# Kernel optimization log

Measured on AMD Instinct MI355X. Metric: run time of the kernel, lower is better.

The kernel has to match this reference:

```python
import jax, jax.numpy as jnp
import numpy as np

B, C, N = 8, 64, 4096
K, M = 20, 8  # neighbors, num_kernel
OUT_C = 64
NEG_SLOPE = 0.2


def setup_inputs() -> dict:
    key = jax.random.key(0)
    k1, k2, k3, k4, k5, k6 = jax.random.split(key, 6)
    x = jax.random.normal(k1, (B, 3, N), dtype=jnp.float32)
    feature = jax.random.normal(k2, (B, C, N), dtype=jnp.float32)
    neigh_indexs = jax.random.randint(k3, (B, N, K), 0, N, dtype=jnp.int64)
    kernels = jax.random.normal(k4, (3, M), dtype=jnp.float32)
    conv_w = jax.random.normal(k5, (OUT_C, C * M), dtype=jnp.float32) * (1.0 / np.sqrt(C * M))
    conv_b = jax.random.normal(k6, (OUT_C,), dtype=jnp.float32) * 0.01
    return {"x": x, "feature": feature, "neigh_indexs": neigh_indexs,
            "kernels": kernels, "conv_w": conv_w, "conv_b": conv_b}


def reference(x, feature, neigh_indexs, kernels, conv_w, conv_b):
    b, c, n = feature.shape
    k = K
    m = kernels.shape[1]
    idx = neigh_indexs[:, :, :k]  # dilation=1 slice, (B,N,K)
    bidx = jnp.arange(b)[:, None, None]

    xt = jnp.transpose(x, (0, 2, 1))            # (B,N,3)
    x_neighs = xt[bidx, idx]                    # (B,N,K,3) irregular gather
    x_rel = x_neighs - x_neighs[:, :, :1, :]    # relative coords to first neighbor

    # kernel projection + one_padding buffer (zeros with [0,0]=1)
    one_pad = jnp.zeros((k, m), dtype=x.dtype).at[0, 0].set(1.0)
    permatrix = jnp.einsum('bnkc,cm->bnkm', x_rel, kernels) + one_pad
    # topkmax: stable softmax over the neighbor axis (soft assignment of
    # neighbors to each of the m kernel slots)
    permatrix = jax.nn.softmax(permatrix, axis=2)  # (B,N,K,M)

    ft = jnp.transpose(feature, (0, 2, 1))      # (B,N,C)
    f_neighs = ft[bidx, idx]                    # (B,N,K,C)
    # feats (B*N,C,K) @ permatrix (B*N,K,M) -> (B*N,C,M); flatten C-major
    agg = jnp.einsum('bnkc,bnkm->bncm', f_neighs, permatrix).reshape(b, n, c * m)

    # BasicConv: 1x1 conv == dense over channel dim, then LeakyReLU(0.2)
    out = agg @ conv_w.T + conv_b               # (B,N,out_c)
    out = jax.nn.leaky_relu(out, NEG_SLOPE)
    out = jnp.transpose(out, (0, 2, 1))         # (B,out_c,N)
    return out + feature                        # residual since in_c == out_c
```

## Files before the change

kernel.cpp:

```cpp
#include <hip/hip_runtime.h>
#include <hip/hip_bf16.h>

#define BB 8
#define CC 64
#define NNN 4096
#define KK 20
#define MM 8
#define OC 64
#define CM 512

typedef __attribute__((ext_vector_type(8))) short bf16x8;
typedef __attribute__((ext_vector_type(4))) float f32x4;
typedef __attribute__((ext_vector_type(2))) float f32x2;

__device__ __forceinline__ unsigned short f2bf(float f) {
    union { float f; unsigned int u; } v; v.f = f;
    unsigned int u = v.u;
    return (unsigned short)((u + 0x7FFFu + ((u >> 16) & 1u)) >> 16);
}
__device__ __forceinline__ unsigned int pack2bf(float a, float b) {
    union { __hip_bfloat162 h; unsigned int u; } pk;
    pk.h = __float22bfloat162_rn(make_float2(a, b));
    return pk.u;
}
__device__ __forceinline__ float bfhi2f(unsigned int u) {
    union { unsigned int u; float f; } v; v.u = u & 0xffff0000u; return v.f;
}
__device__ __forceinline__ float bflo2f(unsigned int u) {
    union { unsigned int u; float f; } v; v.u = u << 16; return v.f;
}

__global__ __launch_bounds__(256) void prep_kernel(const float* __restrict__ x,
                                                   const float* __restrict__ feature,
                                                   const float* __restrict__ kern,
                                                   const float* __restrict__ conv_w,
                                                   unsigned short* __restrict__ ftr,
                                                   unsigned short* __restrict__ Wb,
                                                   float* __restrict__ proj) {
    int blk = blockIdx.x;
    int t = threadIdx.x;
    if (blk < 512) {
        __shared__ float tile[64 * 65];
        int b = blk & 7;
        int n0 = (blk >> 3) << 6;
        const float* fb = feature + b * (CC * NNN);
        #pragma unroll
        for (int s = 0; s < 16; ++s) {
            int i = t + s * 256;
            int c = i >> 6, nn = i & 63;
            tile[c * 65 + nn] = fb[c * NNN + n0 + nn];
        }
        __syncthreads();
        unsigned short* fo = ftr + b * (NNN * CC) + n0 * CC;
        #pragma unroll
        for (int s = 0; s < 16; ++s) {
            int i = t + s * 256;
            int n = i >> 6, cc = i & 63;
            fo[n * CC + cc] = f2bf(tile[cc * 65 + n]);
        }
    } else if (blk < 516) {
        int base = (blk - 512) * 8192;
        #pragma unroll
        for (int s = 0; s < 32; ++s) {
            int i = base + t + s * 256;
            int o = i >> 9, col = i & 511;
            int j = col >> 6, cL = (col >> 3) & 7, m = col & 7;
            int cm = ((cL * 8 + j) << 3) | m;
            Wb[i] = f2bf(conv_w[(o << 9) | cm]);
        }
    } else {
        int pb = blk - 516;
        int b = pb >> 2;
        int nb = (pb & 3) << 10;
        const float* xb = x + b * (3 * NNN);
        float k0[MM], k1[MM], k2[MM];
        #pragma unroll
        for (int m = 0; m < MM; ++m) {
            k0[m] = kern[m]; k1[m] = kern[MM + m]; k2[m] = kern[2 * MM + m];
        }
        #pragma unroll
        for (int s = 0; s < 4; ++s) {
            int n = nb + s * 256 + t;
            float x0 = xb[n], x1 = xb[NNN + n], x2 = xb[2 * NNN + n];
            float pr[MM];
            #pragma unroll
            for (int m = 0; m < MM; ++m)
                pr[m] = x0 * k0[m] + x1 * k1[m] + x2 * k2[m];
            float* pp = proj + ((size_t)b * NNN + n) * MM;
            *(float4*)pp = make_float4(pr[0], pr[1], pr[2], pr[3]);
            *(float4*)(pp + 4) = make_float4(pr[4], pr[5], pr[6], pr[7]);
        }
    }
}

__global__ __launch_bounds__(256, 3) void aggr_kernel(const int* __restrict__ nidx,
                                                      const float* __restrict__ proj,
                                                      const unsigned short* __restrict__ ftr,
                                                      unsigned short* __restrict__ agg) {
    __shared__ unsigned short perm[4][8 * 168];

    int t = threadIdx.x, w = t >> 6, l = t & 63;
    int p = l >> 3, h = l & 7;
    int blk = blockIdx.x;
    int b = blk & 7;
    int n0 = ((blk >> 3) << 5) + (w << 3);
    int rowp = b * NNN + n0 + p;

    int id[KK];
    {
        const int4* nb4 = (const int4*)(nidx + rowp * KK);
        #pragma unroll
        for (int s = 0; s < 5; ++s) {
            int4 v = nb4[s];
            id[s * 4 + 0] = v.x; id[s * 4 + 1] = v.y;
            id[s * 4 + 2] = v.z; id[s * 4 + 3] = v.w;
        }
    }

    const float* pj = proj + (size_t)b * NNN * MM;
    float pv[KK];
    #pragma unroll
    for (int k = 0; k < KK; ++k) pv[k] = pj[id[k] * MM + h];

    const unsigned short* fb = ftr + (size_t)b * NNN * CC;
    uint4 fr[KK];
    #pragma unroll
    for (int k = 0; k < KK; ++k)
        fr[k] = *(const uint4*)(fb + (size_t)id[k] * CC + h * 8);

    float pbase = pv[0];
    #pragma unroll
    for (int k = 0; k < KK; ++k) pv[k] -= pbase;
    if (h == 0) pv[0] += 1.0f;
    float mx = pv[0];
    #pragma unroll
    for (int k = 1; k < KK; ++k) mx = fmaxf(mx, pv[k]);
    float sum = 0.f;
    #pragma unroll
    for (int k = 0; k < KK; ++k) { pv[k] = __expf(pv[k] - mx); sum += pv[k]; }
    float inv = 1.0f / sum;

    {
        unsigned short* pw = perm[w] + p * 168;
        #pragma unroll
        for (int k = 0; k < KK; ++k) pw[k * 8 + h] = f2bf(pv[k] * inv);
    }
    __asm__ __volatile__("s_waitcnt lgkmcnt(0)" ::: "memory");

    f32x2 acc[4][MM];
    #pragma unroll
    for (int d = 0; d < 4; ++d)
        #pragma unroll
        for (int m = 0; m < MM; ++m) acc[d][m] = (f32x2){0.f, 0.f};

    const unsigned short* prd = perm[w] + p * 168;
    #pragma unroll
    for (int k = 0; k < KK; ++k) {
        union { bf16x8 v; unsigned int u[4]; } pm8;
        pm8.v = *(const bf16x8*)(prd + k * 8);
        float pm[MM];
        #pragma unroll
        for (int d = 0; d < 4; ++d) {
            pm[2 * d] = bflo2f(pm8.u[d]);
            pm[2 * d + 1] = bfhi2f(pm8.u[d]);
        }
        const unsigned int* fu = (const unsigned int*)&fr[k];
        f32x2 fv[4];
        #pragma unroll
        for (int d = 0; d < 4; ++d)
            fv[d] = (f32x2){bflo2f(fu[d]), bfhi2f(fu[d])};
        #pragma unroll
        for (int m = 0; m < MM; ++m) {
            f32x2 pmm = {pm[m], pm[m]};
            #pragma unroll
            for (int d = 0; d < 4; ++d)
                acc[d][m] += fv[d] * pmm;
        }
    }

    unsigned short* ag = agg + (size_t)rowp * CM;
    #pragma unroll
    for (int jj = 0; jj < 8; ++jj) {
        int d = jj >> 1;
        unsigned int d0, d1, d2, d3;
        if ((jj & 1) == 0) {
            d0 = pack2bf(acc[d][0].x, acc[d][1].x);
            d1 = pack2bf(acc[d][2].x, acc[d][3].x);
            d2 = pack2bf(acc[d][4].x, acc[d][5].x);
            d3 = pack2bf(acc[d][6].x, acc[d][7].x);
        } else {
            d0 = pack2bf(acc[d][0].y, acc[d][1].y);
            d1 = pack2bf(acc[d][2].y, acc[d][3].y);
            d2 = pack2bf(acc[d][4].y, acc[d][5].y);
            d3 = pack2bf(acc[d][6].y, acc[d][7].y);
        }
        uint4 vv = make_uint4(d0, d1, d2, d3);
        *(uint4*)(ag + jj * 64 + h * 8) = vv;
    }
}

__global__ __launch_bounds__(128, 4) void gemm_kernel(const unsigned short* __restrict__ agg,
                                                      const unsigned short* __restrict__ Wb,
                                                      const float* __restrict__ conv_b,
                                                      const float* __restrict__ feature,
                                                      float* __restrict__ out) {
    int t = threadIdx.x, w = t >> 6, l = t & 63;
    int blk = blockIdx.x;
    int b = blk & 7;
    int g = blk >> 3;
    int Wid = g * 2 + w;
    int og = Wid & 1;
    int pg = Wid >> 1;
    int n0 = pg << 5;
    int oA = og * 32 + (l & 15), oB = oA + 16;
    int q = l >> 4;
    int r0 = b * NNN + n0 + (l & 15);

    const unsigned short* a0p = agg + (size_t)r0 * CM + q * 8;
    const unsigned short* a1p = a0p + 16 * CM;
    const unsigned short* w0p = Wb + (size_t)oA * CM + q * 8;
    const unsigned short* w1p = Wb + (size_t)oB * CM + q * 8;

    const float* fA = feature + ((size_t)b * CC + oA) * NNN + n0 + q * 4;
    const float* fB = feature + ((size_t)b * CC + oB) * NNN + n0 + q * 4;
    float4 resA0 = *(const float4*)fA;
    float4 resA1 = *(const float4*)(fA + 16);
    float4 resB0 = *(const float4*)fB;
    float4 resB1 = *(const float4*)(fB + 16);
    float biasA = conv_b[oA], biasB = conv_b[oB];

    f32x4 d00 = {0,0,0,0}, d01 = {0,0,0,0}, d10 = {0,0,0,0}, d11 = {0,0,0,0};
    #pragma unroll
    for (int s = 0; s < 16; ++s) {
        bf16x8 a0 = *(const bf16x8*)(a0p + s * 32);
        bf16x8 a1 = *(const bf16x8*)(a1p + s * 32);
        bf16x8 w0f = *(const bf16x8*)(w0p + s * 32);
        bf16x8 w1f = *(const bf16x8*)(w1p + s * 32);
        d00 = __builtin_amdgcn_mfma_f32_16x16x32_bf16(a0, w0f, d00, 0, 0, 0);
        d01 = __builtin_amdgcn_mfma_f32_16x16x32_bf16(a0, w1f, d01, 0, 0, 0);
        d10 = __builtin_amdgcn_mfma_f32_16x16x32_bf16(a1, w0f, d10, 0, 0, 0);
        d11 = __builtin_amdgcn_mfma_f32_16x16x32_bf16(a1, w1f, d11, 0, 0, 0);
    }

    float* opA = out + ((size_t)b * OC + oA) * NNN + n0 + q * 4;
    float* opB = out + ((size_t)b * OC + oB) * NNN + n0 + q * 4;
    float4 rA0, rA1, rB0, rB1;
    #pragma unroll
    for (int r = 0; r < 4; ++r) {
        float v;
        v = d00[r] + biasA; v = v > 0.f ? v : v * 0.2f; ((float*)&rA0)[r] = v + ((const float*)&resA0)[r];
        v = d10[r] + biasA; v = v > 0.f ? v : v * 0.2f; ((float*)&rA1)[r] = v + ((const float*)&resA1)[r];
        v = d01[r] + biasB; v = v > 0.f ? v : v * 0.2f; ((float*)&rB0)[r] = v + ((const float*)&resB0)[r];
        v = d11[r] + biasB; v = v > 0.f ? v : v * 0.2f; ((float*)&rB1)[r] = v + ((const float*)&resB1)[r];
    }
    *(float4*)opA = rA0;
    *(float4*)(opA + 16) = rA1;
    *(float4*)opB = rB0;
    *(float4*)(opB + 16) = rB1;
}

extern "C" void kernel_launch(void* const* d_in, const int* in_sizes, int n_in,
                              void* d_out, int out_size, void* d_ws, size_t ws_size,
                              hipStream_t stream) {
    const float* x        = (const float*)d_in[0];
    const float* feature  = (const float*)d_in[1];
    const int*   nidx     = (const int*)d_in[2];
    const float* kern     = (const float*)d_in[3];
    const float* conv_w   = (const float*)d_in[4];
    const float* conv_b   = (const float*)d_in[5];
    float* out = (float*)d_out;

    char* ws = (char*)d_ws;
    unsigned short* ftr  = (unsigned short*)ws;
    unsigned short* Wb   = (unsigned short*)(ws + (4u << 20));
    float*          proj = (float*)(ws + (4u << 20) + (64u << 10));
    unsigned short* agg  = (unsigned short*)(ws + (5u << 20) + (64u << 10));

    prep_kernel<<<548, 256, 0, stream>>>(x, feature, kern, conv_w, ftr, Wb, proj);
    aggr_kernel<<<1024, 256, 0, stream>>>(nidx, proj, ftr, agg);
    gemm_kernel<<<1024, 128, 0, stream>>>(agg, Wb, conv_b, feature, out);
}
```

Before: 120.1 us.

## Fuse neighbor aggregation and output GEMM into one kernel via LDS

Merges the aggregation and MFMA GEMM kernels so each 128-thread block aggregates 16 points into shared memory and immediately runs the 1x1 conv, removing the global round trip of the bf16 aggregate buffer and one launch. It also drops the pbase subtraction (softmax is shift-invariant), restores natural weight column ordering with a matching LDS layout, and double-buffers the neighbor feature gathers in groups of four to cut register pressure. In exchange each block has more serial work and a block barrier, and the weight rows are re-read by every block.

```diff
diff --git a/kernel.cpp b/kernel.cpp
--- a/kernel.cpp
+++ b/kernel.cpp
@@ -8,6 +8,9 @@
 #define MM 8
 #define OC 64
 #define CM 512
+#define PST 168
+#define AST 520
+#define REGW 5504
 
 typedef __attribute__((ext_vector_type(8))) short bf16x8;
 typedef __attribute__((ext_vector_type(4))) float f32x4;
@@ -63,10 +66,7 @@
         #pragma unroll
         for (int s = 0; s < 32; ++s) {
             int i = base + t + s * 256;
-            int o = i >> 9, col = i & 511;
-            int j = col >> 6, cL = (col >> 3) & 7, m = col & 7;
-            int cm = ((cL * 8 + j) << 3) | m;
-            Wb[i] = f2bf(conv_w[(o << 9) | cm]);
+            Wb[i] = f2bf(conv_w[i]);
         }
     } else {
         int pb = blk - 516;
@@ -93,22 +93,30 @@
     }
 }
 
-__global__ __launch_bounds__(256, 3) void aggr_kernel(const int* __restrict__ nidx,
-                                                      const float* __restrict__ proj,
-                                                      const unsigned short* __restrict__ ftr,
-                                                      unsigned short* __restrict__ agg) {
-    __shared__ unsigned short perm[4][8 * 168];
+__global__ __launch_bounds__(128, 3) void main_kernel(
+    const int* __restrict__ nidx,
+    const float* __restrict__ proj,
+    const unsigned short* __restrict__ ftr,
+    const unsigned short* __restrict__ Wb,
+    const float* __restrict__ conv_b,
+    const float* __restrict__ feature,
+    float* __restrict__ out)
+{
+    __shared__ __align__(16) unsigned short sm[2 * REGW];
 
     int t = threadIdx.x, w = t >> 6, l = t & 63;
     int p = l >> 3, h = l & 7;
     int blk = blockIdx.x;
     int b = blk & 7;
-    int n0 = ((blk >> 3) << 5) + (w << 3);
-    int rowp = b * NNN + n0 + p;
+    int n0 = (blk >> 3) << 4;
+    int rowp = b * NNN + n0 + w * 8 + p;
+
+    unsigned short* permW = sm + w * REGW;
+    unsigned short* aggW  = sm + w * REGW + 8 * PST;
 
     int id[KK];
     {
-        const int4* nb4 = (const int4*)(nidx + rowp * KK);
+        const int4* nb4 = (const int4*)(nidx + (size_t)rowp * KK);
         #pragma unroll
         for (int s = 0; s < 5; ++s) {
             int4 v = nb4[s];
@@ -123,14 +131,11 @@
     for (int k = 0; k < KK; ++k) pv[k] = pj[id[k] * MM + h];
 
     const unsigned short* fb = ftr + (size_t)b * NNN * CC;
-    uint4 fr[KK];
-    #pragma unroll
-    for (int k = 0; k < KK; ++k)
-        fr[k] = *(const uint4*)(fb + (size_t)id[k] * CC + h * 8);
-
-    float pbase = pv[0];
-    #pragma unroll
-    for (int k = 0; k < KK; ++k) pv[k] -= pbase;
+    uint4 frA[4], frB[4];
+    #pragma unroll
+    for (int j = 0; j < 4; ++j)
+        frA[j] = *(const uint4*)(fb + (size_t)id[j] * CC + h * 8);
+
     if (h == 0) pv[0] += 1.0f;
     float mx = pv[0];
     #pragma unroll
@@ -141,7 +146,7 @@
     float inv = 1.0f / sum;
 
     {
-        unsigned short* pw = perm[w] + p * 168;
+        unsigned short* pw = permW + p * PST;
         #pragma unroll
         for (int k = 0; k < KK; ++k) pw[k * 8 + h] = f2bf(pv[k] * inv);
     }
@@ -153,110 +158,98 @@
         #pragma unroll
         for (int m = 0; m < MM; ++m) acc[d][m] = (f32x2){0.f, 0.f};
 
-    const unsigned short* prd = perm[w] + p * 168;
-    #pragma unroll
-    for (int k = 0; k < KK; ++k) {
-        union { bf16x8 v; unsigned int u[4]; } pm8;
-        pm8.v = *(const bf16x8*)(prd + k * 8);
-        float pm[MM];
-        #pragma unroll
-        for (int d = 0; d < 4; ++d) {
-            pm[2 * d] = bflo2f(pm8.u[d]);
-            pm[2 * d + 1] = bfhi2f(pm8.u[d]);
-        }
-        const unsigned int* fu = (const unsigned int*)&fr[k];
-        f32x2 fv[4];
-        #pragma unroll
-        for (int d = 0; d < 4; ++d)
-            fv[d] = (f32x2){bflo2f(fu[d]), bfhi2f(fu[d])};
-        #pragma unroll
-        for (int m = 0; m < MM; ++m) {
-            f32x2 pmm = {pm[m], pm[m]};
+    const unsigned short* prd = permW + p * PST;
+    #pragma unroll
+    for (int c4 = 0; c4 < 5; ++c4) {
+        uint4* cur = (c4 & 1) ? frB : frA;
+        uint4* nxt = (c4 & 1) ? frA : frB;
+        if (c4 < 4) {
+            #pragma unroll
+            for (int j = 0; j < 4; ++j)
+                nxt[j] = *(const uint4*)(fb + (size_t)id[(c4 + 1) * 4 + j] * CC + h * 8);
+        }
+        #pragma unroll
+        for (int j = 0; j < 4; ++j) {
+            int k = c4 * 4 + j;
+            union { bf16x8 v; unsigned int u[4]; } pm8;
+            pm8.v = *(const bf16x8*)(prd + k * 8);
+            float pm[MM];
+            #pragma unroll
+            for (int d = 0; d < 4; ++d) {
+                pm[2 * d] = bflo2f(pm8.u[d]);
+                pm[2 * d + 1] = bfhi2f(pm8.u[d]);
+            }
+            const unsigned int* fu = (const unsigned int*)&cur[j];
+            f32x2 fv[4];
             #pragma unroll
             for (int d = 0; d < 4; ++d)
-                acc[d][m] += fv[d] * pmm;
-        }
-    }
-
-    unsigned short* ag = agg + (size_t)rowp * CM;
-    #pragma unroll
-    for (int jj = 0; jj < 8; ++jj) {
-        int d = jj >> 1;
-        unsigned int d0, d1, d2, d3;
-        if ((jj & 1) == 0) {
-            d0 = pack2bf(acc[d][0].x, acc[d][1].x);
-            d1 = pack2bf(acc[d][2].x, acc[d][3].x);
-            d2 = pack2bf(acc[d][4].x, acc[d][5].x);
-            d3 = pack2bf(acc[d][6].x, acc[d][7].x);
-        } else {
-            d0 = pack2bf(acc[d][0].y, acc[d][1].y);
-            d1 = pack2bf(acc[d][2].y, acc[d][3].y);
-            d2 = pack2bf(acc[d][4].y, acc[d][5].y);
-            d3 = pack2bf(acc[d][6].y, acc[d][7].y);
-        }
-        uint4 vv = make_uint4(d0, d1, d2, d3);
-        *(uint4*)(ag + jj * 64 + h * 8) = vv;
-    }
-}
-
-__global__ __launch_bounds__(128, 4) void gemm_kernel(const unsigned short* __restrict__ agg,
-                                                      const unsigned short* __restrict__ Wb,
-                                                      const float* __restrict__ conv_b,
-                                                      const float* __restrict__ feature,
-                                                      float* __restrict__ out) {
-    int t = threadIdx.x, w = t >> 6, l = t & 63;
-    int blk = blockIdx.x;
-    int b = blk & 7;
-    int g = blk >> 3;
-    int Wid = g * 2 + w;
-    int og = Wid & 1;
-    int pg = Wid >> 1;
-    int n0 = pg << 5;
-    int oA = og * 32 + (l & 15), oB = oA + 16;
-    int q = l >> 4;
-    int r0 = b * NNN + n0 + (l & 15);
-
-    const unsigned short* a0p = agg + (size_t)r0 * CM + q * 8;
-    const unsigned short* a1p = a0p + 16 * CM;
-    const unsigned short* w0p = Wb + (size_t)oA * CM + q * 8;
-    const unsigned short* w1p = Wb + (size_t)oB * CM + q * 8;
-
-    const float* fA = feature + ((size_t)b * CC + oA) * NNN + n0 + q * 4;
-    const float* fB = feature + ((size_t)b * CC + oB) * NNN + n0 + q * 4;
-    float4 resA0 = *(const float4*)fA;
-    float4 resA1 = *(const float4*)(fA + 16);
-    float4 resB0 = *(const float4*)fB;
-    float4 resB1 = *(const float4*)(fB + 16);
-    float biasA = conv_b[oA], biasB = conv_b[oB];
-
-    f32x4 d00 = {0,0,0,0}, d01 = {0,0,0,0}, d10 = {0,0,0,0}, d11 = {0,0,0,0};
-    #pragma unroll
-    for (int s = 0; s < 16; ++s) {
-        bf16x8 a0 = *(const bf16x8*)(a0p + s * 32);
-        bf16x8 a1 = *(const bf16x8*)(a1p + s * 32);
-        bf16x8 w0f = *(const bf16x8*)(w0p + s * 32);
-        bf16x8 w1f = *(const bf16x8*)(w1p + s * 32);
-        d00 = __builtin_amdgcn_mfma_f32_16x16x32_bf16(a0, w0f, d00, 0, 0, 0);
-        d01 = __builtin_amdgcn_mfma_f32_16x16x32_bf16(a0, w1f, d01, 0, 0, 0);
-        d10 = __builtin_amdgcn_mfma_f32_16x16x32_bf16(a1, w0f, d10, 0, 0, 0);
-        d11 = __builtin_amdgcn_mfma_f32_16x16x32_bf16(a1, w1f, d11, 0, 0, 0);
-    }
-
-    float* opA = out + ((size_t)b * OC + oA) * NNN + n0 + q * 4;
-    float* opB = out + ((size_t)b * OC + oB) * NNN + n0 + q * 4;
-    float4 rA0, rA1, rB0, rB1;
-    #pragma unroll
-    for (int r = 0; r < 4; ++r) {
-        float v;
-        v = d00[r] + biasA; v = v > 0.f ? v : v * 0.2f; ((float*)&rA0)[r] = v + ((const float*)&resA0)[r];
-        v = d10[r] + biasA; v = v > 0.f ? v : v * 0.2f; ((float*)&rA1)[r] = v + ((const float*)&resA1)[r];
-        v = d01[r] + biasB; v = v > 0.f ? v : v * 0.2f; ((float*)&rB0)[r] = v + ((const float*)&resB0)[r];
-        v = d11[r] + biasB; v = v > 0.f ? v : v * 0.2f; ((float*)&rB1)[r] = v + ((const float*)&resB1)[r];
-    }
-    *(float4*)opA = rA0;
-    *(float4*)(opA + 16) = rA1;
-    *(float4*)opB = rB0;
-    *(float4*)(opB + 16) = rB1;
+                fv[d] = (f32x2){bflo2f(fu[d]), bfhi2f(fu[d])};
+            #pragma unroll
+            for (int m = 0; m < MM; ++m) {
+                f32x2 pmm = {pm[m], pm[m]};
+                #pragma unroll
+                for (int d = 0; d < 4; ++d)
+                    acc[d][m] += fv[d] * pmm;
+            }
+        }
+    }
+
+    {
+        unsigned short* ag = aggW + p * AST;
+        #pragma unroll
+        for (int i = 0; i < 8; ++i) {
+            int d = i >> 1;
+            unsigned int d0, d1, d2, d3;
+            if ((i & 1) == 0) {
+                d0 = pack2bf(acc[d][0].x, acc[d][1].x);
+                d1 = pack2bf(acc[d][2].x, acc[d][3].x);
+                d2 = pack2bf(acc[d][4].x, acc[d][5].x);
+                d3 = pack2bf(acc[d][6].x, acc[d][7].x);
+            } else {
+                d0 = pack2bf(acc[d][0].y, acc[d][1].y);
+                d1 = pack2bf(acc[d][2].y, acc[d][3].y);
+                d2 = pack2bf(acc[d][4].y, acc[d][5].y);
+                d3 = pack2bf(acc[d][6].y, acc[d][7].y);
+            }
+            *(uint4*)(ag + (h * 8 + i) * 8) = make_uint4(d0, d1, d2, d3);
+        }
+    }
+    __syncthreads();
+
+    {
+        int row = l & 15, q = l >> 4;
+        int oA = w * 32 + row, oB = oA + 16;
+        const unsigned short* arow = sm + (row >> 3) * REGW + 8 * PST
+                                     + (row & 7) * AST + q * 8;
+        const unsigned short* wrA = Wb + (size_t)oA * CM + q * 8;
+        const unsigned short* wrB = Wb + (size_t)oB * CM + q * 8;
+        float4 resA = *(const float4*)(feature + ((size_t)b * CC + oA) * NNN + n0 + q * 4);
+        float4 resB = *(const float4*)(feature + ((size_t)b * CC + oB) * NNN + n0 + q * 4);
+        float biasA = conv_b[oA], biasB = conv_b[oB];
+
+        f32x4 dA = {0.f, 0.f, 0.f, 0.f};
+        f32x4 dB = {0.f, 0.f, 0.f, 0.f};
+        #pragma unroll
+        for (int s = 0; s < 16; ++s) {
+            bf16x8 af = *(const bf16x8*)(arow + s * 32);
+            bf16x8 w0 = *(const bf16x8*)(wrA + s * 32);
+            bf16x8 w1 = *(const bf16x8*)(wrB + s * 32);
+            dA = __builtin_amdgcn_mfma_f32_16x16x32_bf16(af, w0, dA, 0, 0, 0);
+            dB = __builtin_amdgcn_mfma_f32_16x16x32_bf16(af, w1, dB, 0, 0, 0);
+        }
+        float4 rA, rB;
+        #pragma unroll
+        for (int r = 0; r < 4; ++r) {
+            float vA = dA[r] + biasA;
+            vA = vA > 0.f ? vA : vA * 0.2f;
+            ((float*)&rA)[r] = vA + ((const float*)&resA)[r];
+            float vB = dB[r] + biasB;
+            vB = vB > 0.f ? vB : vB * 0.2f;
+            ((float*)&rB)[r] = vB + ((const float*)&resB)[r];
+        }
+        *(float4*)(out + ((size_t)b * OC + oA) * NNN + n0 + q * 4) = rA;
+        *(float4*)(out + ((size_t)b * OC + oB) * NNN + n0 + q * 4) = rB;
+    }
 }
 
 extern "C" void kernel_launch(void* const* d_in, const int* in_sizes, int n_in,
@@ -274,9 +267,7 @@
     unsigned short* ftr  = (unsigned short*)ws;
     unsigned short* Wb   = (unsigned short*)(ws + (4u << 20));
     float*          proj = (float*)(ws + (4u << 20) + (64u << 10));
-    unsigned short* agg  = (unsigned short*)(ws + (5u << 20) + (64u << 10));
 
     prep_kernel<<<548, 256, 0, stream>>>(x, feature, kern, conv_w, ftr, Wb, proj);
-    aggr_kernel<<<1024, 256, 0, stream>>>(nidx, proj, ftr, agg);
-    gemm_kernel<<<1024, 128, 0, stream>>>(agg, Wb, conv_b, feature, out);
-}
+    main_kernel<<<2048, 128, 0, stream>>>(nidx, proj, ftr, Wb, conv_b, feature, out);
+}
```

Result: faster. 107.0 us (-10.9%).
